# Kernel optimization log

Hardware: AMD Instinct MI355X
Metric: run time of the kernel (lower is better)

The kernel has to match this reference:

```python
import jax, jax.numpy as jnp
import numpy as np

N, E, IN, C, ED = 100000, 1600000, 128, 64, 16
L, SC, NCL, NM = 3, 256, 2, 4000  # n_conv_layers, classifier width, n_classifier_layers, n_graphs
INV_SQRT_C = 1.0 / np.sqrt(C).astype(np.float32)


def _w(k, shape):
    fan_in = shape[-2] if len(shape) > 1 else shape[-1]
    return jax.random.normal(k, shape, jnp.float32) / np.sqrt(fan_in).astype(np.float32)


def setup_inputs() -> dict:
    key = jax.random.key(0)
    ks = jax.random.split(key, 40)
    inp = {
        "x": jax.random.normal(ks[0], (N, IN), jnp.float32),
        "edge_index": jax.random.randint(ks[1], (2, E), 0, N, jnp.int32),
        "edge_attr": jax.random.normal(ks[2], (E, ED), jnp.float32),
        "batch": jnp.sort(jax.random.randint(ks[3], (N,), 0, NM, jnp.int32)),
        # conv1 (IN -> C), heads=1
        "Wq1": _w(ks[4], (IN, C)), "bq1": jnp.zeros((C,), jnp.float32),
        "Wk1": _w(ks[5], (IN, C)), "bk1": jnp.zeros((C,), jnp.float32),
        "Wv1": _w(ks[6], (IN, C)), "bv1": jnp.zeros((C,), jnp.float32),
        "We1": _w(ks[7], (ED, C)),  # lin_edge has no bias in PyG TransformerConv
        "Ws1": _w(ks[8], (IN, C)), "bs1": jnp.zeros((C,), jnp.float32),
        # stacked conv layers (C -> C)
        "Wq": _w(ks[9], (L, C, C)), "bq": jnp.zeros((L, C), jnp.float32),
        "Wk": _w(ks[10], (L, C, C)), "bk": jnp.zeros((L, C), jnp.float32),
        "Wv": _w(ks[11], (L, C, C)), "bv": jnp.zeros((L, C), jnp.float32),
        "We": _w(ks[12], (L, ED, C)),
        "Ws": _w(ks[13], (L, C, C)), "bs": jnp.zeros((L, C), jnp.float32),
        # classifier head
        "W1": _w(ks[14], (C * (L + 1), SC)), "b1": jnp.zeros((SC,), jnp.float32),
        "Wc": _w(ks[15], (NCL, SC, SC)), "bc": jnp.zeros((NCL, SC), jnp.float32),
        "Wf": _w(ks[16], (SC, 1)), "bf": jnp.zeros((1,), jnp.float32),
    }
    return inp


def _tconv(h, src, dst, ea_proj_in, Wq, bq, Wk, bk, Wv, bv, We, Ws, bs):
    n = h.shape[0]
    q = h @ Wq + bq                      # [N,C]
    k = h @ Wk + bk
    v = h @ Wv + bv
    e = ea_proj_in @ We                  # [E,C]
    ke = k[src] + e                      # gather + edge add
    ve = v[src] + e
    alpha = jnp.sum(q[dst] * ke, axis=-1) * INV_SQRT_C  # [E]
    m = jax.ops.segment_max(alpha, dst, num_segments=n)
    m = jnp.where(jnp.isfinite(m), m, 0.0)
    p = jnp.exp(alpha - m[dst])
    s = jax.ops.segment_sum(p, dst, num_segments=n)
    p = p / (s[dst] + 1e-16)             # PyG-style segment softmax
    out = jax.ops.segment_sum(ve * p[:, None], dst, num_segments=n)
    return out + h @ Ws + bs             # root_weight skip


def reference(x, edge_index, edge_attr, batch,
              Wq1, bq1, Wk1, bk1, Wv1, bv1, We1, Ws1, bs1,
              Wq, bq, Wk, bk, Wv, bv, We, Ws, bs,
              W1, b1, Wc, bc, Wf, bf):
    src, dst = edge_index[0], edge_index[1]
    h = jax.nn.leaky_relu(_tconv(x, src, dst, edge_attr,
                                 Wq1, bq1, Wk1, bk1, Wv1, bv1, We1, Ws1, bs1))
    hs = []
    for i in range(L):
        h = jax.nn.leaky_relu(_tconv(h, src, dst, edge_attr,
                                     Wq[i], bq[i], Wk[i], bk[i], Wv[i], bv[i],
                                     We[i], Ws[i], bs[i]))
        hs.append(h)
    h_pool = jax.ops.segment_sum(h, batch, num_segments=NM)   # global_add_pool
    h_pool_ = h_pool[batch]                                    # repeat_interleave (batch sorted)
    h = jnp.concatenate(hs + [h_pool_], axis=1)                # [N, C*(L+1)]
    h = h @ W1 + b1                                            # no activation before loop (as in source)
    for i in range(NCL):
        h = jax.nn.leaky_relu(h @ Wc[i] + bc[i])
    return jax.nn.sigmoid(h @ Wf + bf)                         # [N,1]
```

## Files before the change

### kernel.cpp

```cpp
#include <hip/hip_runtime.h>
#include <cstdint>
#include <cstddef>

#define NN 100000
#define EE 1600000
#define NMG 4000

__global__ __launch_bounds__(256) void tf_hist(const int* __restrict__ dst, int* __restrict__ deg) {
    int j = blockIdx.x * 256 + threadIdx.x;
    if (j < EE) atomicAdd(&deg[dst[j]], 1);
}

__global__ __launch_bounds__(256) void tf_scan1(const int* __restrict__ deg, int* __restrict__ rp,
                                                int* __restrict__ part) {
    __shared__ int sm[256];
    int tid = threadIdx.x;
    int i = blockIdx.x * 256 + tid;
    int v = (i < NN) ? deg[i] : 0;
    sm[tid] = v;
    __syncthreads();
    for (int off = 1; off < 256; off <<= 1) {
        int t = (tid >= off) ? sm[tid - off] : 0;
        __syncthreads();
        sm[tid] += t;
        __syncthreads();
    }
    if (i < NN) rp[i] = sm[tid] - v;
    if (tid == 255) part[blockIdx.x] = sm[255];
}

__global__ __launch_bounds__(512) void tf_scan2(const int* __restrict__ part, int* __restrict__ offs, int nb) {
    __shared__ int sm[512];
    int tid = threadIdx.x;
    int v = (tid < nb) ? part[tid] : 0;
    sm[tid] = v;
    __syncthreads();
    for (int off = 1; off < 512; off <<= 1) {
        int t = (tid >= off) ? sm[tid - off] : 0;
        __syncthreads();
        sm[tid] += t;
        __syncthreads();
    }
    if (tid < nb) offs[tid] = sm[tid] - v;
}

__global__ __launch_bounds__(256) void tf_scan3(int* __restrict__ rp, const int* __restrict__ offs) {
    int i = blockIdx.x * 256 + threadIdx.x;
    if (i < NN) rp[i] += offs[i >> 8];
    else if (i == NN) rp[NN] = EE;
}

__global__ __launch_bounds__(256) void tf_scatter(const int* __restrict__ src, const int* __restrict__ dst,
                                                  const int* __restrict__ rp, int* __restrict__ cur,
                                                  int* __restrict__ ssrc, int* __restrict__ seid) {
    int j = blockIdx.x * 256 + threadIdx.x;
    if (j >= EE) return;
    int d = dst[j];
    int pos = atomicAdd(&cur[d], 1);
    int slot = rp[d] + pos;
    ssrc[slot] = src[j];
    seid[slot] = j;
}

__global__ __launch_bounds__(256) void tf_ecopy(const int* __restrict__ seid, const float* __restrict__ ea,
                                                float* __restrict__ eac) {
    size_t idx = (size_t)blockIdx.x * 256 + threadIdx.x;
    if (idx >= (size_t)EE * 4) return;
    size_t slot = idx >> 2;
    int c4 = (int)(idx & 3);
    const float4* srcp = (const float4*)(ea + (size_t)seid[slot] * 16);
    ((float4*)(eac + slot * 16))[c4] = srcp[c4];
}

template <int MODE>
__global__ __launch_bounds__(256) void tf_gemm(
    const float* __restrict__ A,
    const float* __restrict__ hs0, const float* __restrict__ hs1,
    const float* __restrict__ hs2, const float* __restrict__ pl,
    const int* __restrict__ batch,
    const float* __restrict__ W0, const float* __restrict__ W1p,
    const float* __restrict__ W2, const float* __restrict__ W3,
    const float* __restrict__ b0, const float* __restrict__ b1p,
    const float* __restrict__ b2, const float* __restrict__ b3,
    float* __restrict__ O0, float* __restrict__ O1,
    float* __restrict__ O2, float* __restrict__ O3,
    int Kdim, int act) {
    __shared__ float As[64][17];
    __shared__ float Bs[16][256];
    int tid = threadIdx.x;
    int tx = tid & 15, ty = tid >> 4;
    int bm = blockIdx.x * 64;
    int tx4 = tx * 4;
    float acc[4][16];
#pragma unroll
    for (int j = 0; j < 4; ++j)
#pragma unroll
        for (int i = 0; i < 16; ++i) acc[j][i] = 0.f;

    int arow = tid >> 2;
    int aq = (tid & 3) * 4;
    int grow = bm + arow;

    for (int k0 = 0; k0 < Kdim; k0 += 16) {
        float4 av = make_float4(0.f, 0.f, 0.f, 0.f);
        if (grow < NN) {
            if (MODE == 1) {
                int k = k0 + aq, g = k >> 6, c = k & 63;
                if (g == 3) av = *(const float4*)(pl + (size_t)batch[grow] * 64 + c);
                else {
                    const float* s = (g == 0) ? hs0 : (g == 1) ? hs1 : hs2;
                    av = *(const float4*)(s + (size_t)grow * 64 + c);
                }
            } else {
                av = *(const float4*)(A + (size_t)grow * Kdim + k0 + aq);
            }
        }
        As[arow][aq + 0] = av.x; As[arow][aq + 1] = av.y;
        As[arow][aq + 2] = av.z; As[arow][aq + 3] = av.w;
#pragma unroll
        for (int r = 0; r < 4; ++r) {
            int f4 = tid + r * 256;
            int t = f4 >> 6;
            int col = (f4 & 63) * 4;
            float4 bv;
            if (MODE == 0) {
                int g = col >> 6, c = col & 63;
                const float* Wg = (g == 0) ? W0 : (g == 1) ? W1p : (g == 2) ? W2 : W3;
                bv = *(const float4*)(Wg + (size_t)(k0 + t) * 64 + c);
            } else {
                bv = *(const float4*)(W0 + (size_t)(k0 + t) * 256 + col);
            }
            *(float4*)&Bs[t][col] = bv;
        }
        __syncthreads();
#pragma unroll
        for (int t = 0; t < 16; ++t) {
            float a0 = As[ty * 4 + 0][t], a1 = As[ty * 4 + 1][t];
            float a2 = As[ty * 4 + 2][t], a3 = As[ty * 4 + 3][t];
            float4 v0 = *(const float4*)&Bs[t][tx4 + 0];
            float4 v1 = *(const float4*)&Bs[t][tx4 + 64];
            float4 v2 = *(const float4*)&Bs[t][tx4 + 128];
            float4 v3 = *(const float4*)&Bs[t][tx4 + 192];
            float bb[16] = {v0.x, v0.y, v0.z, v0.w, v1.x, v1.y, v1.z, v1.w,
                            v2.x, v2.y, v2.z, v2.w, v3.x, v3.y, v3.z, v3.w};
#pragma unroll
            for (int i = 0; i < 16; ++i) {
                acc[0][i] = fmaf(a0, bb[i], acc[0][i]);
                acc[1][i] = fmaf(a1, bb[i], acc[1][i]);
                acc[2][i] = fmaf(a2, bb[i], acc[2][i]);
                acc[3][i] = fmaf(a3, bb[i], acc[3][i]);
            }
        }
        __syncthreads();
    }
    if (MODE == 0) {
#pragma unroll
        for (int g = 0; g < 4; ++g) {
            const float* bias = (g == 0) ? b0 : (g == 1) ? b1p : (g == 2) ? b2 : b3;
            float* Out = (g == 0) ? O0 : (g == 1) ? O1 : (g == 2) ? O2 : O3;
            float4 bv = *(const float4*)(bias + tx4);
#pragma unroll
            for (int j = 0; j < 4; ++j) {
                int r = bm + ty * 4 + j;
                if (r < NN) {
                    float4 v;
                    v.x = acc[j][g * 4 + 0] + bv.x;
                    v.y = acc[j][g * 4 + 1] + bv.y;
                    v.z = acc[j][g * 4 + 2] + bv.z;
                    v.w = acc[j][g * 4 + 3] + bv.w;
                    *(float4*)(Out + (size_t)r * 64 + tx4) = v;
                }
            }
        }
    } else {
#pragma unroll
        for (int j = 0; j < 4; ++j) {
            int r = bm + ty * 4 + j;
            if (r < NN) {
#pragma unroll
                for (int g = 0; g < 4; ++g) {
                    int col = tx4 + g * 64;
                    float4 v;
                    v.x = acc[j][g * 4 + 0] + b0[col + 0];
                    v.y = acc[j][g * 4 + 1] + b0[col + 1];
                    v.z = acc[j][g * 4 + 2] + b0[col + 2];
                    v.w = acc[j][g * 4 + 3] + b0[col + 3];
                    if (act) {
                        v.x = v.x > 0.f ? v.x : 0.01f * v.x;
                        v.y = v.y > 0.f ? v.y : 0.01f * v.y;
                        v.z = v.z > 0.f ? v.z : 0.01f * v.z;
                        v.w = v.w > 0.f ? v.w : 0.01f * v.w;
                    }
                    *(float4*)(O0 + (size_t)r * 256 + col) = v;
                }
            }
        }
    }
}

template <bool USE_EAC>
__global__ __launch_bounds__(256) void tf_agg(
    const float* __restrict__ Q, const float* __restrict__ Km,
    const float* __restrict__ V, const float* __restrict__ BASE,
    const int* __restrict__ rp, const int* __restrict__ ssrc, const int* __restrict__ seid,
    const float* __restrict__ eaw,
    const float* __restrict__ We,
    float* __restrict__ out) {
    __shared__ float qsm[4][64];
    int wv = threadIdx.x >> 6;
    int node = (blockIdx.x << 2) + wv;
    int lane = threadIdx.x & 63;
    if (node >= NN) return;

    float q = Q[(size_t)node * 64 + lane];

    qsm[wv][lane] = q;
    int dgrp = lane >> 2;
    int cb = lane & 3;
    float pq = 0.f;
#pragma unroll
    for (int k2 = 0; k2 < 16; ++k2) {
        int c = cb + (k2 << 2);
        pq = fmaf(qsm[wv][c], We[dgrp * 64 + c], pq);
    }
    pq += __shfl_xor(pq, 1);
    pq += __shfl_xor(pq, 2);
    float qel = __shfl(pq, (lane & 15) << 2);

    int beg = rp[node], end = rp[node + 1];
    float s = 0.f, acc = 0.f, pea = 0.f;

    int it = beg;
    for (; it + 3 < end; it += 4) {
        int s0 = ssrc[it], s1 = ssrc[it + 1], s2 = ssrc[it + 2], s3 = ssrc[it + 3];
        float ea0, ea1, ea2, ea3;
        if (USE_EAC) {
            ea0 = (lane < 16) ? eaw[(size_t)it * 16 + lane] : 0.f;
            ea1 = (lane < 16) ? eaw[(size_t)(it + 1) * 16 + lane] : 0.f;
            ea2 = (lane < 16) ? eaw[(size_t)(it + 2) * 16 + lane] : 0.f;
            ea3 = (lane < 16) ? eaw[(size_t)(it + 3) * 16 + lane] : 0.f;
        } else {
            int j0 = seid[it], j1 = seid[it + 1], j2 = seid[it + 2], j3 = seid[it + 3];
            ea0 = (lane < 16) ? eaw[(size_t)j0 * 16 + lane] : 0.f;
            ea1 = (lane < 16) ? eaw[(size_t)j1 * 16 + lane] : 0.f;
            ea2 = (lane < 16) ? eaw[(size_t)j2 * 16 + lane] : 0.f;
            ea3 = (lane < 16) ? eaw[(size_t)j3 * 16 + lane] : 0.f;
        }
        float k0 = Km[(size_t)s0 * 64 + lane];
        float k1 = Km[(size_t)s1 * 64 + lane];
        float k2 = Km[(size_t)s2 * 64 + lane];
        float k3 = Km[(size_t)s3 * 64 + lane];
        float v0 = V[(size_t)s0 * 64 + lane];
        float v1 = V[(size_t)s1 * 64 + lane];
        float v2 = V[(size_t)s2 * 64 + lane];
        float v3 = V[(size_t)s3 * 64 + lane];
        float p0 = fmaf(q, k0, ea0 * qel);
        float p1 = fmaf(q, k1, ea1 * qel);
        float p2 = fmaf(q, k2, ea2 * qel);
        float p3 = fmaf(q, k3, ea3 * qel);
#pragma unroll
        for (int o = 32; o; o >>= 1) {
            p0 += __shfl_xor(p0, o);
            p1 += __shfl_xor(p1, o);
            p2 += __shfl_xor(p2, o);
            p3 += __shfl_xor(p3, o);
        }
        float e0 = __expf(p0 * 0.125f);
        float e1 = __expf(p1 * 0.125f);
        float e2 = __expf(p2 * 0.125f);
        float e3 = __expf(p3 * 0.125f);
        s += (e0 + e1) + (e2 + e3);
        acc = fmaf(e0, v0, fmaf(e1, v1, fmaf(e2, v2, fmaf(e3, v3, acc))));
        pea = fmaf(e0, ea0, fmaf(e1, ea1, fmaf(e2, ea2, fmaf(e3, ea3, pea))));
    }
    for (; it < end; ++it) {
        int s0 = ssrc[it];
        float ea0;
        if (USE_EAC) ea0 = (lane < 16) ? eaw[(size_t)it * 16 + lane] : 0.f;
        else {
            int j0 = seid[it];
            ea0 = (lane < 16) ? eaw[(size_t)j0 * 16 + lane] : 0.f;
        }
        float k0 = Km[(size_t)s0 * 64 + lane];
        float v0 = V[(size_t)s0 * 64 + lane];
        float p0 = fmaf(q, k0, ea0 * qel);
#pragma unroll
        for (int o = 32; o; o >>= 1) p0 += __shfl_xor(p0, o);
        float e0 = __expf(p0 * 0.125f);
        s += e0;
        acc = fmaf(e0, v0, acc);
        pea = fmaf(e0, ea0, pea);
    }

    float base = BASE[(size_t)node * 64 + lane];
    float o;
    if (end > beg) {
        float eaout = 0.f;
#pragma unroll
        for (int d = 0; d < 16; ++d) eaout = fmaf(__shfl(pea, d), We[d * 64 + lane], eaout);
        o = (acc + eaout) / (s + 1e-16f) + base;
    } else {
        o = base;
    }
    out[(size_t)node * 64 + lane] = (o > 0.f) ? o : 0.01f * o;
}

__global__ __launch_bounds__(256) void tf_pool(const float* __restrict__ h, const int* __restrict__ bat,
                                               float* __restrict__ pl) {
    int idx = blockIdx.x * 256 + threadIdx.x;
    if (idx >= NN * 64) return;
    int node = idx >> 6, l = idx & 63;
    atomicAdd(&pl[(size_t)bat[node] * 64 + l], h[idx]);
}

__global__ __launch_bounds__(256) void tf_final(const float* __restrict__ g, const float* __restrict__ Wf,
                                                const float* __restrict__ bf, float* __restrict__ out) {
    int wid = (blockIdx.x * 256 + threadIdx.x) >> 6;
    int lane = threadIdx.x & 63;
    if (wid >= NN) return;
    const float* row = g + (size_t)wid * 256;
    float s = row[lane] * Wf[lane] + row[lane + 64] * Wf[lane + 64] +
              row[lane + 128] * Wf[lane + 128] + row[lane + 192] * Wf[lane + 192];
#pragma unroll
    for (int off = 32; off; off >>= 1) s += __shfl_xor(s, off);
    if (lane == 0) out[wid] = 1.f / (1.f + __expf(-(s + bf[0])));
}

extern "C" void kernel_launch(void* const* d_in, const int* in_sizes, int n_in,
                              void* d_out, int out_size, void* d_ws, size_t ws_size,
                              hipStream_t stream) {
    (void)in_sizes; (void)n_in; (void)out_size;
    const float* x   = (const float*)d_in[0];
    const int*   ei  = (const int*)d_in[1];
    const float* ea  = (const float*)d_in[2];
    const int*   bat = (const int*)d_in[3];
    const float* Wq1 = (const float*)d_in[4];  const float* bq1 = (const float*)d_in[5];
    const float* Wk1 = (const float*)d_in[6];  const float* bk1 = (const float*)d_in[7];
    const float* Wv1 = (const float*)d_in[8];  const float* bv1 = (const float*)d_in[9];
    const float* We1 = (const float*)d_in[10];
    const float* Ws1 = (const float*)d_in[11]; const float* bs1 = (const float*)d_in[12];
    const float* WqL = (const float*)d_in[13]; const float* bqL = (const float*)d_in[14];
    const float* WkL = (const float*)d_in[15]; const float* bkL = (const float*)d_in[16];
    const float* WvL = (const float*)d_in[17]; const float* bvL = (const float*)d_in[18];
    const float* WeL = (const float*)d_in[19];
    const float* WsL = (const float*)d_in[20]; const float* bsL = (const float*)d_in[21];
    const float* W1  = (const float*)d_in[22]; const float* b1  = (const float*)d_in[23];
    const float* Wc  = (const float*)d_in[24]; const float* bc  = (const float*)d_in[25];
    const float* Wf  = (const float*)d_in[26]; const float* bf  = (const float*)d_in[27];
    float* outp = (float*)d_out;

    char* ws = (char*)d_ws;
    size_t off = 0;
    auto carve = [&](size_t bytes) {
        char* p = ws + off;
        off = (off + bytes + 255) & ~(size_t)255;
        return p;
    };
    int* rp    = (int*)carve((NN + 1) * sizeof(int));
    int* cur   = (int*)carve((size_t)NN * sizeof(int));
    int* part  = (int*)carve(512 * sizeof(int));
    int* offs  = (int*)carve(512 * sizeof(int));
    int* ssrc  = (int*)carve((size_t)EE * sizeof(int));
    int* seid  = (int*)carve((size_t)EE * sizeof(int));
    float* bigA = (float*)carve((size_t)NN * 256 * sizeof(float));
    float* bigB = (float*)carve((size_t)NN * 256 * sizeof(float));
    float* pl   = (float*)carve((size_t)NMG * 64 * sizeof(float));
    const size_t EAC_BYTES = (size_t)EE * 16 * sizeof(float);
    bool use_eac = (off + EAC_BYTES) <= ws_size;
    float* eac = use_eac ? (float*)carve(EAC_BYTES) : nullptr;

    float* Q    = bigA;
    float* Km   = bigA + (size_t)NN * 64;
    float* V    = bigA + (size_t)NN * 128;
    float* BASE = bigA + (size_t)NN * 192;
    float* h0   = bigB;
    float* hA   = bigB + (size_t)NN * 64;
    float* hB   = bigB + (size_t)NN * 128;
    float* hC   = bigB + (size_t)NN * 192;
    float* g1 = bigA;
    float* g2 = bigB;
    float* g3 = bigA;

    const int* esrc = ei;
    const int* edst = ei + EE;

    hipMemsetAsync(cur, 0, (size_t)NN * sizeof(int), stream);
    tf_hist<<<EE / 256, 256, 0, stream>>>(edst, cur);
    tf_scan1<<<391, 256, 0, stream>>>(cur, rp, part);
    tf_scan2<<<1, 512, 0, stream>>>(part, offs, 391);
    tf_scan3<<<392, 256, 0, stream>>>(rp, offs);
    hipMemsetAsync(cur, 0, (size_t)NN * sizeof(int), stream);
    tf_scatter<<<EE / 256, 256, 0, stream>>>(esrc, edst, rp, cur, ssrc, seid);
    if (use_eac)
        tf_ecopy<<<(EE * 4) / 256, 256, 0, stream>>>(seid, ea, eac);

    const int GB = (NN + 63) / 64;
    const int AB = NN / 4;

    tf_gemm<0><<<GB, 256, 0, stream>>>(x, nullptr, nullptr, nullptr, nullptr, nullptr,
                                       Wq1, Wk1, Wv1, Ws1, bq1, bk1, bv1, bs1,
                                       Q, Km, V, BASE, 128, 0);
    if (use_eac)
        tf_agg<true><<<AB, 256, 0, stream>>>(Q, Km, V, BASE, rp, ssrc, seid, eac, We1, h0);
    else
        tf_agg<false><<<AB, 256, 0, stream>>>(Q, Km, V, BASE, rp, ssrc, seid, ea, We1, h0);

    const float* hin = h0;
    float* houts[3] = {hA, hB, hC};
    for (int l = 0; l < 3; ++l) {
        tf_gemm<0><<<GB, 256, 0, stream>>>(hin, nullptr, nullptr, nullptr, nullptr, nullptr,
                                           WqL + l * 4096, WkL + l * 4096, WvL + l * 4096, WsL + l * 4096,
                                           bqL + l * 64, bkL + l * 64, bvL + l * 64, bsL + l * 64,
                                           Q, Km, V, BASE, 64, 0);
        if (use_eac)
            tf_agg<true><<<AB, 256, 0, stream>>>(Q, Km, V, BASE, rp, ssrc, seid, eac,
                                                 WeL + l * 1024, houts[l]);
        else
            tf_agg<false><<<AB, 256, 0, stream>>>(Q, Km, V, BASE, rp, ssrc, seid, ea,
                                                  WeL + l * 1024, houts[l]);
        hin = houts[l];
    }

    hipMemsetAsync(pl, 0, (size_t)NMG * 64 * sizeof(float), stream);
    tf_pool<<<AB, 256, 0, stream>>>(hC, bat, pl);

    tf_gemm<1><<<GB, 256, 0, stream>>>(nullptr, hA, hB, hC, pl, bat,
                                       W1, nullptr, nullptr, nullptr,
                                       b1, nullptr, nullptr, nullptr,
                                       g1, nullptr, nullptr, nullptr, 256, 0);
    tf_gemm<2><<<GB, 256, 0, stream>>>(g1, nullptr, nullptr, nullptr, nullptr, nullptr,
                                       Wc, nullptr, nullptr, nullptr,
                                       bc, nullptr, nullptr, nullptr,
                                       g2, nullptr, nullptr, nullptr, 256, 1);
    tf_gemm<2><<<GB, 256, 0, stream>>>(g2, nullptr, nullptr, nullptr, nullptr, nullptr,
                                       Wc + 65536, nullptr, nullptr, nullptr,
                                       bc + 256, nullptr, nullptr, nullptr,
                                       g3, nullptr, nullptr, nullptr, 256, 1);
    tf_final<<<AB, 256, 0, stream>>>(g3, Wf, bf, outp);
}
```

Before: 1.869 ms.

## Fuse final sigmoid head into last classifier GEMM and transpose A tile

The last classifier GEMM gains a MODE 3 epilogue that applies bias, leaky-ReLU, the dot product with Wf, an in-block shared-memory reduction and the sigmoid. This removes the separate tf_final kernel and the write and re-read of the 100000x256 intermediate. The A tile is now stored transposed in shared memory so each k-step reads a float4 of four rows, and non-MODE-0 GEMMs use a K-step of 32 instead of 16. The larger tile raises shared-memory use per block, which may lower occupancy.

```diff
diff --git a/kernel.cpp b/kernel.cpp
--- a/kernel.cpp
+++ b/kernel.cpp
@@ -84,9 +84,11 @@
     const float* __restrict__ b2, const float* __restrict__ b3,
     float* __restrict__ O0, float* __restrict__ O1,
     float* __restrict__ O2, float* __restrict__ O3,
+    const float* __restrict__ Wfp, const float* __restrict__ bfp,
     int Kdim, int act) {
-    __shared__ float As[64][17];
-    __shared__ float Bs[16][256];
+    constexpr int BKv = (MODE == 0) ? 16 : 32;
+    __shared__ float Ast[BKv][68];
+    __shared__ float Bs[BKv][256];
     int tid = threadIdx.x;
     int tx = tid & 15, ty = tid >> 4;
     int bm = blockIdx.x * 64;
@@ -97,28 +99,31 @@
 #pragma unroll
         for (int i = 0; i < 16; ++i) acc[j][i] = 0.f;
 
-    int arow = tid >> 2;
-    int aq = (tid & 3) * 4;
-    int grow = bm + arow;
-
-    for (int k0 = 0; k0 < Kdim; k0 += 16) {
-        float4 av = make_float4(0.f, 0.f, 0.f, 0.f);
-        if (grow < NN) {
-            if (MODE == 1) {
-                int k = k0 + aq, g = k >> 6, c = k & 63;
-                if (g == 3) av = *(const float4*)(pl + (size_t)batch[grow] * 64 + c);
-                else {
-                    const float* s = (g == 0) ? hs0 : (g == 1) ? hs1 : hs2;
-                    av = *(const float4*)(s + (size_t)grow * 64 + c);
+    for (int k0 = 0; k0 < Kdim; k0 += BKv) {
+#pragma unroll
+        for (int r = 0; r < BKv / 16; ++r) {
+            int f4 = tid + r * 256;
+            int row = f4 / (BKv / 4);
+            int q4 = (f4 % (BKv / 4)) * 4;
+            int grow = bm + row;
+            float4 av = make_float4(0.f, 0.f, 0.f, 0.f);
+            if (grow < NN) {
+                if (MODE == 1) {
+                    int k = k0 + q4, g = k >> 6, c = k & 63;
+                    if (g == 3) av = *(const float4*)(pl + (size_t)batch[grow] * 64 + c);
+                    else {
+                        const float* s = (g == 0) ? hs0 : (g == 1) ? hs1 : hs2;
+                        av = *(const float4*)(s + (size_t)grow * 64 + c);
+                    }
+                } else {
+                    av = *(const float4*)(A + (size_t)grow * Kdim + k0 + q4);
                 }
-            } else {
-                av = *(const float4*)(A + (size_t)grow * Kdim + k0 + aq);
-            }
-        }
-        As[arow][aq + 0] = av.x; As[arow][aq + 1] = av.y;
-        As[arow][aq + 2] = av.z; As[arow][aq + 3] = av.w;
-#pragma unroll
-        for (int r = 0; r < 4; ++r) {
+            }
+            Ast[q4 + 0][row] = av.x; Ast[q4 + 1][row] = av.y;
+            Ast[q4 + 2][row] = av.z; Ast[q4 + 3][row] = av.w;
+        }
+#pragma unroll
+        for (int r = 0; r < BKv / 4; ++r) {
             int f4 = tid + r * 256;
             int t = f4 >> 6;
             int col = (f4 & 63) * 4;
@@ -133,10 +138,9 @@
             *(float4*)&Bs[t][col] = bv;
         }
         __syncthreads();
-#pragma unroll
-        for (int t = 0; t < 16; ++t) {
-            float a0 = As[ty * 4 + 0][t], a1 = As[ty * 4 + 1][t];
-            float a2 = As[ty * 4 + 2][t], a3 = As[ty * 4 + 3][t];
+#pragma unroll 8
+        for (int t = 0; t < BKv; ++t) {
+            float4 a4 = *(const float4*)&Ast[t][ty * 4];
             float4 v0 = *(const float4*)&Bs[t][tx4 + 0];
             float4 v1 = *(const float4*)&Bs[t][tx4 + 64];
             float4 v2 = *(const float4*)&Bs[t][tx4 + 128];
@@ -145,10 +149,10 @@
                             v2.x, v2.y, v2.z, v2.w, v3.x, v3.y, v3.z, v3.w};
 #pragma unroll
             for (int i = 0; i < 16; ++i) {
-                acc[0][i] = fmaf(a0, bb[i], acc[0][i]);
-                acc[1][i] = fmaf(a1, bb[i], acc[1][i]);
-                acc[2][i] = fmaf(a2, bb[i], acc[2][i]);
-                acc[3][i] = fmaf(a3, bb[i], acc[3][i]);
+                acc[0][i] = fmaf(a4.x, bb[i], acc[0][i]);
+                acc[1][i] = fmaf(a4.y, bb[i], acc[1][i]);
+                acc[2][i] = fmaf(a4.z, bb[i], acc[2][i]);
+                acc[3][i] = fmaf(a4.w, bb[i], acc[3][i]);
             }
         }
         __syncthreads();
@@ -171,6 +175,39 @@
                     *(float4*)(Out + (size_t)r * 64 + tx4) = v;
                 }
             }
+        }
+    } else if (MODE == 3) {
+        float4 wfv[4];
+#pragma unroll
+        for (int g = 0; g < 4; ++g) wfv[g] = *(const float4*)(Wfp + tx4 + g * 64);
+        float part[4];
+#pragma unroll
+        for (int j = 0; j < 4; ++j) {
+            part[j] = 0.f;
+#pragma unroll
+            for (int g = 0; g < 4; ++g) {
+                int col = tx4 + g * 64;
+                float x0 = acc[j][g * 4 + 0] + b0[col + 0];
+                float x1 = acc[j][g * 4 + 1] + b0[col + 1];
+                float x2 = acc[j][g * 4 + 2] + b0[col + 2];
+                float x3 = acc[j][g * 4 + 3] + b0[col + 3];
+                x0 = x0 > 0.f ? x0 : 0.01f * x0;
+                x1 = x1 > 0.f ? x1 : 0.01f * x1;
+                x2 = x2 > 0.f ? x2 : 0.01f * x2;
+                x3 = x3 > 0.f ? x3 : 0.01f * x3;
+                part[j] += x0 * wfv[g].x + x1 * wfv[g].y + x2 * wfv[g].z + x3 * wfv[g].w;
+            }
+        }
+        float* red = &Bs[0][0];
+#pragma unroll
+        for (int j = 0; j < 4; ++j) red[(ty * 4 + j) * 17 + tx] = part[j];
+        __syncthreads();
+        if (tid < 64) {
+            float s = 0.f;
+#pragma unroll
+            for (int i = 0; i < 16; ++i) s += red[tid * 17 + i];
+            int r = bm + tid;
+            if (r < NN) O0[r] = 1.f / (1.f + __expf(-(s + bfp[0])));
         }
     } else {
 #pragma unroll
@@ -203,8 +240,7 @@
     const float* __restrict__ Q, const float* __restrict__ Km,
     const float* __restrict__ V, const float* __restrict__ BASE,
     const int* __restrict__ rp, const int* __restrict__ ssrc, const int* __restrict__ seid,
-    const float* __restrict__ eaw,
-    const float* __restrict__ We,
+    const float* __restrict__ eaw, const float* __restrict__ We,
     float* __restrict__ out) {
     __shared__ float qsm[4][64];
     int wv = threadIdx.x >> 6;
@@ -311,19 +347,6 @@
     if (idx >= NN * 64) return;
     int node = idx >> 6, l = idx & 63;
     atomicAdd(&pl[(size_t)bat[node] * 64 + l], h[idx]);
-}
-
-__global__ __launch_bounds__(256) void tf_final(const float* __restrict__ g, const float* __restrict__ Wf,
-                                                const float* __restrict__ bf, float* __restrict__ out) {
-    int wid = (blockIdx.x * 256 + threadIdx.x) >> 6;
-    int lane = threadIdx.x & 63;
-    if (wid >= NN) return;
-    const float* row = g + (size_t)wid * 256;
-    float s = row[lane] * Wf[lane] + row[lane + 64] * Wf[lane + 64] +
-              row[lane + 128] * Wf[lane + 128] + row[lane + 192] * Wf[lane + 192];
-#pragma unroll
-    for (int off = 32; off; off >>= 1) s += __shfl_xor(s, off);
-    if (lane == 0) out[wid] = 1.f / (1.f + __expf(-(s + bf[0])));
 }
 
 extern "C" void kernel_launch(void* const* d_in, const int* in_sizes, int n_in,
@@ -379,7 +402,6 @@
     float* hC   = bigB + (size_t)NN * 192;
     float* g1 = bigA;
     float* g2 = bigB;
-    float* g3 = bigA;
 
     const int* esrc = ei;
     const int* edst = ei + EE;
@@ -399,7 +421,7 @@
 
     tf_gemm<0><<<GB, 256, 0, stream>>>(x, nullptr, nullptr, nullptr, nullptr, nullptr,
                                        Wq1, Wk1, Wv1, Ws1, bq1, bk1, bv1, bs1,
-                                       Q, Km, V, BASE, 128, 0);
+                                       Q, Km, V, BASE, nullptr, nullptr, 128, 0);
     if (use_eac)
         tf_agg<true><<<AB, 256, 0, stream>>>(Q, Km, V, BASE, rp, ssrc, seid, eac, We1, h0);
     else
@@ -411,7 +433,7 @@
         tf_gemm<0><<<GB, 256, 0, stream>>>(hin, nullptr, nullptr, nullptr, nullptr, nullptr,
                                            WqL + l * 4096, WkL + l * 4096, WvL + l * 4096, WsL + l * 4096,
                                            bqL + l * 64, bkL + l * 64, bvL + l * 64, bsL + l * 64,
-                                           Q, Km, V, BASE, 64, 0);
+                                           Q, Km, V, BASE, nullptr, nullptr, 64, 0);
         if (use_eac)
             tf_agg<true><<<AB, 256, 0, stream>>>(Q, Km, V, BASE, rp, ssrc, seid, eac,
                                                  WeL + l * 1024, houts[l]);
@@ -427,14 +449,16 @@
     tf_gemm<1><<<GB, 256, 0, stream>>>(nullptr, hA, hB, hC, pl, bat,
                                        W1, nullptr, nullptr, nullptr,
                                        b1, nullptr, nullptr, nullptr,
-                                       g1, nullptr, nullptr, nullptr, 256, 0);
+                                       g1, nullptr, nullptr, nullptr,
+                                       nullptr, nullptr, 256, 0);
     tf_gemm<2><<<GB, 256, 0, stream>>>(g1, nullptr, nullptr, nullptr, nullptr, nullptr,
                                        Wc, nullptr, nullptr, nullptr,
                                        bc, nullptr, nullptr, nullptr,
-                                       g2, nullptr, nullptr, nullptr, 256, 1);
-    tf_gemm<2><<<GB, 256, 0, stream>>>(g2, nullptr, nullptr, nullptr, nullptr, nullptr,
+                                       g2, nullptr, nullptr, nullptr,
+                                       nullptr, nullptr, 256, 1);
+    tf_gemm<3><<<GB, 256, 0, stream>>>(g2, nullptr, nullptr, nullptr, nullptr, nullptr,
                                        Wc + 65536, nullptr, nullptr, nullptr,
                                        bc + 256, nullptr, nullptr, nullptr,
-                                       g3, nullptr, nullptr, nullptr, 256, 1);
-    tf_final<<<AB, 256, 0, stream>>>(g3, Wf, bf, outp);
-}
+                                       outp, nullptr, nullptr, nullptr,
+                                       Wf, bf, 256, 1);
+}
```

Result: no change. 1.875 ms (+0.3%).
